# Performance work log

Hardware: AMD Instinct MI355X
Metric: run time of the kernel (lower is better)

Reference implementation:

```python
import jax, jax.numpy as jnp
import numpy as np

P = 64  # number of parameters per grid cell
# torch.combinations(param, 2, with_replacement=True) enumerates (i,j) with i<=j
# in row-major order, which matches np.triu_indices.
IDX_I, IDX_J = np.triu_indices(P)  # each length C = P*(P+1)//2 = 2080


def setup_inputs() -> dict:
    key = jax.random.key(0)
    k1, k2 = jax.random.split(key)
    # [B, G1, G2, P]
    param_tensor = jax.random.normal(k1, (32, 64, 64, P), dtype=jnp.float32)
    # [G1, G2, C]
    coeffs = jax.random.normal(k2, (64, 64, len(IDX_I)), dtype=jnp.float32)
    return {"param_tensor": param_tensor, "coeffs": coeffs}


def reference(param_tensor, coeffs):
    # Pairwise products with replacement: p_i * p_j for i <= j  -> [B,G1,G2,C]
    pair = param_tensor[..., IDX_I] * param_tensor[..., IDX_J]
    # Per-cell weighted sum over combinations, then sum over the 2D grid -> [B]
    cell = jnp.einsum('bijc,ijc->bij', pair, coeffs)
    return cell.sum(axis=(1, 2))
```

## Files before the change

kernel.cpp:

```cpp
#include <hip/hip_runtime.h>

#define NP     64
#define NC     2080
#define NCELLS 4096
#define NB     32
#define CELLS_PER_BLOCK 4
#define BLOCKS (NCELLS / CELLS_PER_BLOCK)

typedef short bf16x8  __attribute__((ext_vector_type(8)));
typedef short short4v __attribute__((ext_vector_type(4)));
typedef float f32x16  __attribute__((ext_vector_type(16)));

__device__ __forceinline__ short f2bf(float f) {
  unsigned u = __float_as_uint(f);
  u += 0x7fffu + ((u >> 16) & 1u);
  return (short)(u >> 16);
}

__device__ __forceinline__ int swz(int j, int i) { return i ^ ((j & 15) << 2); }

template <int CTRL>
__device__ __forceinline__ float ror_add(float v) {
  int t = __builtin_amdgcn_update_dpp(0, __float_as_int(v), CTRL, 0xf, 0xf, true);
  return v + __int_as_float(t);
}

__global__ __launch_bounds__(256, 4) void poly_mfma_kernel(
    const float* __restrict__ param,
    const float* __restrict__ coeffs,
    float* __restrict__ ws) {
  __shared__ __align__(16) short scoefT[CELLS_PER_BLOCK][NP][NP];
  __shared__ float sred[CELLS_PER_BLOCK][NB];

  const int tid  = threadIdx.x;
  const int wave = tid >> 6;
  const int lane = tid & 63;
  const int lo5  = lane & 31;
  const int hi   = lane >> 5;
  const int cell = blockIdx.x * CELLS_PER_BLOCK + wave;

  {
    int4* z = reinterpret_cast<int4*>(&scoefT[wave][0][0]);
    const int4 zero = {0, 0, 0, 0};
#pragma unroll
    for (int k = 0; k < 8; ++k) z[k * 64 + lane] = zero;
  }

  {
    const float4* gsrc =
        reinterpret_cast<const float4*>(coeffs + (size_t)cell * NC);
#pragma unroll
    for (int k = 0; k < 9; ++k) {
      const int idx = k * 64 + lane;
      if (idx < NC / 4) {
        const float4 v = gsrc[idx];
        const int c = idx * 4;
        const float fs = sqrtf((float)(16641 - 8 * c));
        int i = (int)((129.0f - fs) * 0.5f);
        int bi = 64 * i - ((i * (i - 1)) >> 1);
        if (c < bi) { --i; bi -= (64 - i); }
        else if (c >= bi + (64 - i)) { bi += (64 - i); ++i; }
        int off = c - bi;
        const float vals[4] = {v.x, v.y, v.z, v.w};
#pragma unroll
        for (int d = 0; d < 4; ++d) {
          const int j = i + off;
          scoefT[wave][j][swz(j, i)] = f2bf(vals[d]);
          ++off;
          if (off == 64 - i) { ++i; off = 0; }
        }
      }
    }
  }

  const float* pb = param + ((size_t)lo5 * NCELLS + cell) * NP;
  bf16x8 afrag[4];
#pragma unroll
  for (int ks = 0; ks < 4; ++ks) {
#pragma unroll
    for (int eh = 0; eh < 2; ++eh) {
      const int i0 = ks * 16 + 4 * hi + 8 * eh;
      const float4 v = *reinterpret_cast<const float4*>(pb + i0);
      afrag[ks][eh * 4 + 0] = f2bf(v.x);
      afrag[ks][eh * 4 + 1] = f2bf(v.y);
      afrag[ks][eh * 4 + 2] = f2bf(v.z);
      afrag[ks][eh * 4 + 3] = f2bf(v.w);
    }
  }

  float pepi0[16], pepi1[16];
#pragma unroll
  for (int r = 0; r < 16; ++r) {
    const int b = (r & 3) + 8 * (r >> 2) + 4 * hi;
    const float* pe = param + ((size_t)b * NCELLS + cell) * NP;
    pepi0[r] = pe[lo5];
    pepi1[r] = pe[lo5 + 32];
  }

  const short* swT = &scoefT[wave][0][0];
  const int jb0 = lo5 * NP;
  const int jb1 = (lo5 + 32) * NP;
  f32x16 acc0, acc1;
#pragma unroll
  for (int r = 0; r < 16; ++r) { acc0[r] = 0.f; acc1[r] = 0.f; }

#pragma unroll
  for (int ks = 0; ks < 4; ++ks) {
    const int ia = ks * 16 + 4 * hi;
    const int ib = ia + 8;
    const short4v a0 = *reinterpret_cast<const short4v*>(swT + jb0 + swz(lo5, ia));
    const short4v a1 = *reinterpret_cast<const short4v*>(swT + jb0 + swz(lo5, ib));
    const short4v c0 = *reinterpret_cast<const short4v*>(swT + jb1 + swz(lo5, ia));
    const short4v c1 = *reinterpret_cast<const short4v*>(swT + jb1 + swz(lo5, ib));
    const bf16x8 b0 = __builtin_shufflevector(a0, a1, 0, 1, 2, 3, 4, 5, 6, 7);
    const bf16x8 b1 = __builtin_shufflevector(c0, c1, 0, 1, 2, 3, 4, 5, 6, 7);
    acc0 = __builtin_amdgcn_mfma_f32_32x32x16_bf16(afrag[ks], b0, acc0, 0, 0, 0);
    acc1 = __builtin_amdgcn_mfma_f32_32x32x16_bf16(afrag[ks], b1, acc1, 0, 0, 0);
  }

#pragma unroll
  for (int r = 0; r < 16; ++r) {
    float v = fmaf(acc0[r], pepi0[r], acc1[r] * pepi1[r]);
    v = ror_add<0x121>(v);
    v = ror_add<0x122>(v);
    v = ror_add<0x124>(v);
    v = ror_add<0x128>(v);
    v += __int_as_float(__builtin_amdgcn_ds_swizzle(__float_as_int(v), 0x401F));
    if (lo5 == 0) {
      const int b = (r & 3) + 8 * (r >> 2) + 4 * hi;
      sred[wave][b] = v;
    }
  }
  __syncthreads();
  if (tid < NB) {
    ws[(size_t)tid * BLOCKS + blockIdx.x] =
        sred[0][tid] + sred[1][tid] + sred[2][tid] + sred[3][tid];
  }
}

__global__ void poly_reduce_kernel(const float* __restrict__ ws,
                                   float* __restrict__ out) {
  const int b = blockIdx.x;
  const int tid = threadIdx.x;
  const float4 v =
      reinterpret_cast<const float4*>(ws + (size_t)b * BLOCKS)[tid];
  float s = (v.x + v.y) + (v.z + v.w);
#pragma unroll
  for (int off = 1; off <= 32; off <<= 1) s += __shfl_xor(s, off, 64);
  __shared__ float sp[4];
  if ((tid & 63) == 0) sp[tid >> 6] = s;
  __syncthreads();
  if (tid == 0) out[b] = (sp[0] + sp[1]) + (sp[2] + sp[3]);
}

extern "C" void kernel_launch(void* const* d_in, const int* in_sizes, int n_in,
                              void* d_out, int out_size, void* d_ws,
                              size_t ws_size, hipStream_t stream) {
  const float* param = (const float*)d_in[0];
  const float* coeffs = (const float*)d_in[1];
  float* out = (float*)d_out;
  float* ws = (float*)d_ws;

  hipLaunchKernelGGL(poly_mfma_kernel, dim3(BLOCKS), dim3(256), 0, stream,
                     param, coeffs, ws);
  hipLaunchKernelGGL(poly_reduce_kernel, dim3(NB), dim3(256), 0, stream, ws,
                     out);
}
```

Baseline: 21.69 us.

## Process two cells per wave and issue global loads before LDS scatter

Each wave now handles two grid cells in sequence instead of one, which halves the grid to 512 blocks. The per-wave partial sums are accumulated in registers across both cells before the block reduction. The coefficient and parameter global loads are now all issued up front into registers before the bf16 scatter into LDS, to expose more memory-level parallelism. The second reduce kernel is resized to 128 threads to match. The trade-offs are fewer resident waves to hide memory latency and higher register pressure from the staged loads.

```diff
diff --git a/kernel.cpp b/kernel.cpp
--- a/kernel.cpp
+++ b/kernel.cpp
@@ -4,8 +4,8 @@
 #define NC     2080
 #define NCELLS 4096
 #define NB     32
-#define CELLS_PER_BLOCK 4
-#define BLOCKS (NCELLS / CELLS_PER_BLOCK)
+#define CELLS_PER_BLOCK 8
+#define TOTALB (NCELLS / CELLS_PER_BLOCK)
 
 typedef short bf16x8  __attribute__((ext_vector_type(8)));
 typedef short short4v __attribute__((ext_vector_type(4)));
@@ -29,15 +29,14 @@
     const float* __restrict__ param,
     const float* __restrict__ coeffs,
     float* __restrict__ ws) {
-  __shared__ __align__(16) short scoefT[CELLS_PER_BLOCK][NP][NP];
-  __shared__ float sred[CELLS_PER_BLOCK][NB];
+  __shared__ __align__(16) short scoefT[4][NP][NP];
+  __shared__ float sred[4][NB];
 
   const int tid  = threadIdx.x;
   const int wave = tid >> 6;
   const int lane = tid & 63;
   const int lo5  = lane & 31;
   const int hi   = lane >> 5;
-  const int cell = blockIdx.x * CELLS_PER_BLOCK + wave;
 
   {
     int4* z = reinterpret_cast<int4*>(&scoefT[wave][0][0]);
@@ -46,22 +45,40 @@
     for (int k = 0; k < 8; ++k) z[k * 64 + lane] = zero;
   }
 
-  {
+  float accred[16];
+#pragma unroll
+  for (int r = 0; r < 16; ++r) accred[r] = 0.f;
+
+  for (int cc = 0; cc < 2; ++cc) {
+    const int cell = blockIdx.x * CELLS_PER_BLOCK + wave * 2 + cc;
+
     const float4* gsrc =
         reinterpret_cast<const float4*>(coeffs + (size_t)cell * NC);
+    float4 cv[9];
+#pragma unroll
+    for (int k = 0; k < 8; ++k) cv[k] = gsrc[k * 64 + lane];
+    if (lane < 8) cv[8] = gsrc[512 + lane];
+
+    const float* pb = param + ((size_t)lo5 * NCELLS + cell) * NP;
+    float4 av[8];
+#pragma unroll
+    for (int ks = 0; ks < 4; ++ks)
+#pragma unroll
+      for (int eh = 0; eh < 2; ++eh)
+        av[ks * 2 + eh] =
+            *reinterpret_cast<const float4*>(pb + ks * 16 + 4 * hi + 8 * eh);
+
 #pragma unroll
     for (int k = 0; k < 9; ++k) {
-      const int idx = k * 64 + lane;
-      if (idx < NC / 4) {
-        const float4 v = gsrc[idx];
-        const int c = idx * 4;
+      if (k < 8 || lane < 8) {
+        const int c = (k * 64 + lane) * 4;
         const float fs = sqrtf((float)(16641 - 8 * c));
         int i = (int)((129.0f - fs) * 0.5f);
         int bi = 64 * i - ((i * (i - 1)) >> 1);
         if (c < bi) { --i; bi -= (64 - i); }
         else if (c >= bi + (64 - i)) { bi += (64 - i); ++i; }
         int off = c - bi;
-        const float vals[4] = {v.x, v.y, v.z, v.w};
+        const float vals[4] = {cv[k].x, cv[k].y, cv[k].z, cv[k].w};
 #pragma unroll
         for (int d = 0; d < 4; ++d) {
           const int j = i + off;
@@ -71,69 +88,71 @@
         }
       }
     }
-  }
 
-  const float* pb = param + ((size_t)lo5 * NCELLS + cell) * NP;
-  bf16x8 afrag[4];
+    bf16x8 afrag[4];
 #pragma unroll
-  for (int ks = 0; ks < 4; ++ks) {
+    for (int ks = 0; ks < 4; ++ks)
 #pragma unroll
-    for (int eh = 0; eh < 2; ++eh) {
-      const int i0 = ks * 16 + 4 * hi + 8 * eh;
-      const float4 v = *reinterpret_cast<const float4*>(pb + i0);
-      afrag[ks][eh * 4 + 0] = f2bf(v.x);
-      afrag[ks][eh * 4 + 1] = f2bf(v.y);
-      afrag[ks][eh * 4 + 2] = f2bf(v.z);
-      afrag[ks][eh * 4 + 3] = f2bf(v.w);
+      for (int eh = 0; eh < 2; ++eh) {
+        const float4 v = av[ks * 2 + eh];
+        afrag[ks][eh * 4 + 0] = f2bf(v.x);
+        afrag[ks][eh * 4 + 1] = f2bf(v.y);
+        afrag[ks][eh * 4 + 2] = f2bf(v.z);
+        afrag[ks][eh * 4 + 3] = f2bf(v.w);
+      }
+
+    float pepi0[16], pepi1[16];
+#pragma unroll
+    for (int r = 0; r < 16; ++r) {
+      const int b = (r & 3) + 8 * (r >> 2) + 4 * hi;
+      const float* pe = param + ((size_t)b * NCELLS + cell) * NP;
+      pepi0[r] = pe[lo5];
+      pepi1[r] = pe[lo5 + 32];
+    }
+
+    const short* swT = &scoefT[wave][0][0];
+    const int jb0 = lo5 * NP;
+    const int jb1 = (lo5 + 32) * NP;
+    f32x16 acc0, acc1;
+#pragma unroll
+    for (int r = 0; r < 16; ++r) { acc0[r] = 0.f; acc1[r] = 0.f; }
+
+#pragma unroll
+    for (int ks = 0; ks < 4; ++ks) {
+      const int ia = ks * 16 + 4 * hi;
+      const int ib = ia + 8;
+      const short4v a0 = *reinterpret_cast<const short4v*>(swT + jb0 + swz(lo5, ia));
+      const short4v a1 = *reinterpret_cast<const short4v*>(swT + jb0 + swz(lo5, ib));
+      const short4v c0 = *reinterpret_cast<const short4v*>(swT + jb1 + swz(lo5, ia));
+      const short4v c1 = *reinterpret_cast<const short4v*>(swT + jb1 + swz(lo5, ib));
+      const bf16x8 b0 = __builtin_shufflevector(a0, a1, 0, 1, 2, 3, 4, 5, 6, 7);
+      const bf16x8 b1 = __builtin_shufflevector(c0, c1, 0, 1, 2, 3, 4, 5, 6, 7);
+      acc0 = __builtin_amdgcn_mfma_f32_32x32x16_bf16(afrag[ks], b0, acc0, 0, 0, 0);
+      acc1 = __builtin_amdgcn_mfma_f32_32x32x16_bf16(afrag[ks], b1, acc1, 0, 0, 0);
+    }
+
+#pragma unroll
+    for (int r = 0; r < 16; ++r) {
+      float v = fmaf(acc0[r], pepi0[r], acc1[r] * pepi1[r]);
+      v = ror_add<0x121>(v);
+      v = ror_add<0x122>(v);
+      v = ror_add<0x124>(v);
+      v = ror_add<0x128>(v);
+      v += __int_as_float(__builtin_amdgcn_ds_swizzle(__float_as_int(v), 0x401F));
+      accred[r] += v;
     }
   }
 
-  float pepi0[16], pepi1[16];
+  if (lo5 == 0) {
 #pragma unroll
-  for (int r = 0; r < 16; ++r) {
-    const int b = (r & 3) + 8 * (r >> 2) + 4 * hi;
-    const float* pe = param + ((size_t)b * NCELLS + cell) * NP;
-    pepi0[r] = pe[lo5];
-    pepi1[r] = pe[lo5 + 32];
-  }
-
-  const short* swT = &scoefT[wave][0][0];
-  const int jb0 = lo5 * NP;
-  const int jb1 = (lo5 + 32) * NP;
-  f32x16 acc0, acc1;
-#pragma unroll
-  for (int r = 0; r < 16; ++r) { acc0[r] = 0.f; acc1[r] = 0.f; }
-
-#pragma unroll
-  for (int ks = 0; ks < 4; ++ks) {
-    const int ia = ks * 16 + 4 * hi;
-    const int ib = ia + 8;
-    const short4v a0 = *reinterpret_cast<const short4v*>(swT + jb0 + swz(lo5, ia));
-    const short4v a1 = *reinterpret_cast<const short4v*>(swT + jb0 + swz(lo5, ib));
-    const short4v c0 = *reinterpret_cast<const short4v*>(swT + jb1 + swz(lo5, ia));
-    const short4v c1 = *reinterpret_cast<const short4v*>(swT + jb1 + swz(lo5, ib));
-    const bf16x8 b0 = __builtin_shufflevector(a0, a1, 0, 1, 2, 3, 4, 5, 6, 7);
-    const bf16x8 b1 = __builtin_shufflevector(c0, c1, 0, 1, 2, 3, 4, 5, 6, 7);
-    acc0 = __builtin_amdgcn_mfma_f32_32x32x16_bf16(afrag[ks], b0, acc0, 0, 0, 0);
-    acc1 = __builtin_amdgcn_mfma_f32_32x32x16_bf16(afrag[ks], b1, acc1, 0, 0, 0);
-  }
-
-#pragma unroll
-  for (int r = 0; r < 16; ++r) {
-    float v = fmaf(acc0[r], pepi0[r], acc1[r] * pepi1[r]);
-    v = ror_add<0x121>(v);
-    v = ror_add<0x122>(v);
-    v = ror_add<0x124>(v);
-    v = ror_add<0x128>(v);
-    v += __int_as_float(__builtin_amdgcn_ds_swizzle(__float_as_int(v), 0x401F));
-    if (lo5 == 0) {
+    for (int r = 0; r < 16; ++r) {
       const int b = (r & 3) + 8 * (r >> 2) + 4 * hi;
-      sred[wave][b] = v;
+      sred[wave][b] = accred[r];
     }
   }
   __syncthreads();
   if (tid < NB) {
-    ws[(size_t)tid * BLOCKS + blockIdx.x] =
+    ws[(size_t)tid * TOTALB + blockIdx.x] =
         sred[0][tid] + sred[1][tid] + sred[2][tid] + sred[3][tid];
   }
 }
@@ -143,14 +162,14 @@
   const int b = blockIdx.x;
   const int tid = threadIdx.x;
   const float4 v =
-      reinterpret_cast<const float4*>(ws + (size_t)b * BLOCKS)[tid];
+      reinterpret_cast<const float4*>(ws + (size_t)b * TOTALB)[tid];
   float s = (v.x + v.y) + (v.z + v.w);
 #pragma unroll
   for (int off = 1; off <= 32; off <<= 1) s += __shfl_xor(s, off, 64);
-  __shared__ float sp[4];
+  __shared__ float sp[2];
   if ((tid & 63) == 0) sp[tid >> 6] = s;
   __syncthreads();
-  if (tid == 0) out[b] = (sp[0] + sp[1]) + (sp[2] + sp[3]);
+  if (tid == 0) out[b] = sp[0] + sp[1];
 }
 
 extern "C" void kernel_launch(void* const* d_in, const int* in_sizes, int n_in,
@@ -161,8 +180,8 @@
   float* out = (float*)d_out;
   float* ws = (float*)d_ws;
 
-  hipLaunchKernelGGL(poly_mfma_kernel, dim3(BLOCKS), dim3(256), 0, stream,
+  hipLaunchKernelGGL(poly_mfma_kernel, dim3(TOTALB), dim3(256), 0, stream,
                      param, coeffs, ws);
-  hipLaunchKernelGGL(poly_reduce_kernel, dim3(NB), dim3(256), 0, stream, ws,
+  hipLaunchKernelGGL(poly_reduce_kernel, dim3(NB), dim3(128), 0, stream, ws,
                      out);
 }
```

Result: slower. 38.70 us (+78.5%).

## Stage param tile through LDS with coalesced loads and hoist coefficient loads

Applied to the files above, without the earlier changes.

Each block now loads its 4 cells × 32 batches of params with fully coalesced float4 loads, converts them to bf16 once, and stores them in shared memory. Both the MFMA A fragments and the epilogue multipliers are then read from LDS, which replaces the strided per-lane global gathers. Coefficient loads are issued up front into registers so they overlap with the param loads. The trade-offs are an extra block-wide barrier, about 16KB more LDS, higher register pressure, and epilogue multipliers that are now rounded to bf16 instead of kept in fp32.

```diff
diff --git a/kernel.cpp b/kernel.cpp
--- a/kernel.cpp
+++ b/kernel.cpp
@@ -6,6 +6,7 @@
 #define NB     32
 #define CELLS_PER_BLOCK 4
 #define BLOCKS (NCELLS / CELLS_PER_BLOCK)
+#define SPSTRIDE 260
 
 typedef short bf16x8  __attribute__((ext_vector_type(8)));
 typedef short short4v __attribute__((ext_vector_type(4)));
@@ -15,6 +16,9 @@
   unsigned u = __float_as_uint(f);
   u += 0x7fffu + ((u >> 16) & 1u);
   return (short)(u >> 16);
+}
+__device__ __forceinline__ float bf2f(short h) {
+  return __uint_as_float(((unsigned)(unsigned short)h) << 16);
 }
 
 __device__ __forceinline__ int swz(int j, int i) { return i ^ ((j & 15) << 2); }
@@ -30,6 +34,7 @@
     const float* __restrict__ coeffs,
     float* __restrict__ ws) {
   __shared__ __align__(16) short scoefT[CELLS_PER_BLOCK][NP][NP];
+  __shared__ __align__(16) short sparam[NB][SPSTRIDE];
   __shared__ float sred[CELLS_PER_BLOCK][NB];
 
   const int tid  = threadIdx.x;
@@ -37,7 +42,8 @@
   const int lane = tid & 63;
   const int lo5  = lane & 31;
   const int hi   = lane >> 5;
-  const int cell = blockIdx.x * CELLS_PER_BLOCK + wave;
+  const int cellbase = blockIdx.x * CELLS_PER_BLOCK;
+  const int cell = cellbase + wave;
 
   {
     int4* z = reinterpret_cast<int4*>(&scoefT[wave][0][0]);
@@ -46,55 +52,62 @@
     for (int k = 0; k < 8; ++k) z[k * 64 + lane] = zero;
   }
 
-  {
-    const float4* gsrc =
-        reinterpret_cast<const float4*>(coeffs + (size_t)cell * NC);
+  const float4* gsrc =
+      reinterpret_cast<const float4*>(coeffs + (size_t)cell * NC);
+  float4 cv[9];
 #pragma unroll
-    for (int k = 0; k < 9; ++k) {
-      const int idx = k * 64 + lane;
-      if (idx < NC / 4) {
-        const float4 v = gsrc[idx];
-        const int c = idx * 4;
-        const float fs = sqrtf((float)(16641 - 8 * c));
-        int i = (int)((129.0f - fs) * 0.5f);
-        int bi = 64 * i - ((i * (i - 1)) >> 1);
-        if (c < bi) { --i; bi -= (64 - i); }
-        else if (c >= bi + (64 - i)) { bi += (64 - i); ++i; }
-        int off = c - bi;
-        const float vals[4] = {v.x, v.y, v.z, v.w};
+  for (int k = 0; k < 8; ++k) cv[k] = gsrc[k * 64 + lane];
+  if (lane < 8) cv[8] = gsrc[512 + lane];
+
+  const float4* pg = reinterpret_cast<const float4*>(param);
+  float4 pv[8];
 #pragma unroll
-        for (int d = 0; d < 4; ++d) {
-          const int j = i + off;
-          scoefT[wave][j][swz(j, i)] = f2bf(vals[d]);
-          ++off;
-          if (off == 64 - i) { ++i; off = 0; }
-        }
+  for (int r = 0; r < 8; ++r) {
+    const int b = r * 4 + wave;
+    pv[r] = pg[((size_t)b * NCELLS + cellbase) * (NP / 4) + lane];
+  }
+
+#pragma unroll
+  for (int k = 0; k < 9; ++k) {
+    if (k < 8 || lane < 8) {
+      const int c = (k * 64 + lane) * 4;
+      const float fs = sqrtf((float)(16641 - 8 * c));
+      int i = (int)((129.0f - fs) * 0.5f);
+      int bi = 64 * i - ((i * (i - 1)) >> 1);
+      if (c < bi) { --i; bi -= (64 - i); }
+      else if (c >= bi + (64 - i)) { bi += (64 - i); ++i; }
+      int off = c - bi;
+      const float vals[4] = {cv[k].x, cv[k].y, cv[k].z, cv[k].w};
+#pragma unroll
+      for (int d = 0; d < 4; ++d) {
+        const int j = i + off;
+        scoefT[wave][j][swz(j, i)] = f2bf(vals[d]);
+        ++off;
+        if (off == 64 - i) { ++i; off = 0; }
       }
     }
   }
 
-  const float* pb = param + ((size_t)lo5 * NCELLS + cell) * NP;
+#pragma unroll
+  for (int r = 0; r < 8; ++r) {
+    const int b = r * 4 + wave;
+    short4v h;
+    h[0] = f2bf(pv[r].x);
+    h[1] = f2bf(pv[r].y);
+    h[2] = f2bf(pv[r].z);
+    h[3] = f2bf(pv[r].w);
+    *reinterpret_cast<short4v*>(&sparam[b][lane * 4]) = h;
+  }
+  __syncthreads();
+
+  const short* sp = &sparam[lo5][wave * NP];
   bf16x8 afrag[4];
 #pragma unroll
   for (int ks = 0; ks < 4; ++ks) {
-#pragma unroll
-    for (int eh = 0; eh < 2; ++eh) {
-      const int i0 = ks * 16 + 4 * hi + 8 * eh;
-      const float4 v = *reinterpret_cast<const float4*>(pb + i0);
-      afrag[ks][eh * 4 + 0] = f2bf(v.x);
-      afrag[ks][eh * 4 + 1] = f2bf(v.y);
-      afrag[ks][eh * 4 + 2] = f2bf(v.z);
-      afrag[ks][eh * 4 + 3] = f2bf(v.w);
-    }
-  }
-
-  float pepi0[16], pepi1[16];
-#pragma unroll
-  for (int r = 0; r < 16; ++r) {
-    const int b = (r & 3) + 8 * (r >> 2) + 4 * hi;
-    const float* pe = param + ((size_t)b * NCELLS + cell) * NP;
-    pepi0[r] = pe[lo5];
-    pepi1[r] = pe[lo5 + 32];
+    const short4v g1 = *reinterpret_cast<const short4v*>(sp + ks * 16 + 4 * hi);
+    const short4v g2 =
+        *reinterpret_cast<const short4v*>(sp + ks * 16 + 4 * hi + 8);
+    afrag[ks] = __builtin_shufflevector(g1, g2, 0, 1, 2, 3, 4, 5, 6, 7);
   }
 
   const short* swT = &scoefT[wave][0][0];
@@ -120,16 +133,16 @@
 
 #pragma unroll
   for (int r = 0; r < 16; ++r) {
-    float v = fmaf(acc0[r], pepi0[r], acc1[r] * pepi1[r]);
+    const int b = (r & 3) + 8 * (r >> 2) + 4 * hi;
+    const float p0 = bf2f(sparam[b][wave * NP + lo5]);
+    const float p1 = bf2f(sparam[b][wave * NP + lo5 + 32]);
+    float v = fmaf(acc0[r], p0, acc1[r] * p1);
     v = ror_add<0x121>(v);
     v = ror_add<0x122>(v);
     v = ror_add<0x124>(v);
     v = ror_add<0x128>(v);
     v += __int_as_float(__builtin_amdgcn_ds_swizzle(__float_as_int(v), 0x401F));
-    if (lo5 == 0) {
-      const int b = (r & 3) + 8 * (r >> 2) + 4 * hi;
-      sred[wave][b] = v;
-    }
+    if (lo5 == 0) sred[wave][b] = v;
   }
   __syncthreads();
   if (tid < NB) {
```

Measured after the change: 21.84 us. No clear change (+0.7%).
